# Kernel tuning notes

Hardware: AMD Instinct MI355X
Metric: run time of the kernel (lower is better)

Reference implementation:

```python
import jax, jax.numpy as jnp
import numpy as np
from jax import lax

B, h, Ch = 16, 8, 32
HW = 56
N = HW * HW
SPLITS = [64, 96, 96]  # [2*Ch, 3*Ch, 3*Ch] for windows {3,5,7}


def _dwconv(x, w, b, pad):
    # x: [B, C, H, W]; w: [C, 1, k, k] depthwise (feature_group_count=C)
    y = lax.conv_general_dilated(
        x, w, window_strides=(1, 1), padding=[(pad, pad), (pad, pad)],
        feature_group_count=x.shape[1],
        dimension_numbers=('NCHW', 'OIHW', 'NCHW'))
    return y + b[None, :, None, None]


def setup_inputs() -> dict:
    key = jax.random.key(0)
    ks = jax.random.split(key, 6)
    return {
        'q': jax.random.normal(ks[0], (B, h, N, Ch), dtype=jnp.float32),
        'v': jax.random.normal(ks[1], (B, h, N, Ch), dtype=jnp.float32),
        'w3': jax.random.normal(ks[2], (64, 1, 3, 3), dtype=jnp.float32) * 0.1,
        'b3': jnp.zeros((64,), dtype=jnp.float32),
        'w5': jax.random.normal(ks[3], (96, 1, 5, 5), dtype=jnp.float32) * 0.1,
        'b5': jnp.zeros((96,), dtype=jnp.float32),
        'w7': jax.random.normal(ks[4], (96, 1, 7, 7), dtype=jnp.float32) * 0.1,
        'b7': jnp.zeros((96,), dtype=jnp.float32),
        'H': HW,
        'W': HW,
    }


def reference(q, v, w3, b3, w5, b5, w7, b7, H, W):
    # q, v: [B, h, N, Ch]; N == H*W, Nv == N (same-resolution path, no interpolation)
    Bq, hh, Nq, C = q.shape
    # v: B h (H W) Ch -> B (h*Ch) H W
    v_img = jnp.transpose(v, (0, 1, 3, 2)).reshape(Bq, hh * C, H, W)
    v1, v2, v3 = jnp.split(v_img, np.cumsum(SPLITS)[:-1], axis=1)
    conv_v = jnp.concatenate([
        _dwconv(v1, w3, b3, 1),
        _dwconv(v2, w5, b5, 2),
        _dwconv(v3, w7, b7, 3),
    ], axis=1)  # [B, h*Ch, H, W]
    # B (h*Ch) H W -> B h (H W) Ch
    conv_v = conv_v.reshape(Bq, hh, C, H * W).transpose(0, 1, 3, 2)
    ev = q * conv_v  # [B, h, N, Ch]
    # transpose(1,2).flatten(2): [B, N, h*Ch]
    return jnp.transpose(ev, (0, 2, 1, 3)).reshape(Bq, Nq, hh * C)
```

## Files before the change

### kernel.cpp

```cpp
#include <hip/hip_runtime.h>
#include <cstddef>


#define BH 16
#define NH 8
#define CH 32
#define HW 56
#define NN (HW*HW)
#define ROWB (HW*CH*4)
#define RS 58
#define NROWS_MAX 20
#define BUF_PX (3 + NROWS_MAX*RS + 1)
#define BUF_FLOATS (BUF_PX*CH)

typedef float f32x4 __attribute__((ext_vector_type(4)));
typedef unsigned int u32x4 __attribute__((ext_vector_type(4)));

__device__ __forceinline__ f32x4 bload(__amdgpu_buffer_rsrc_t rs, int voff) {
    u32x4 u = __builtin_amdgcn_raw_buffer_load_b128(rs, voff, 0, 0);
    f32x4 f; __builtin_memcpy(&f, &u, 16); return f;
}

template<int K, int R>
__device__ __forceinline__ void conv_rows(
    const float* __restrict__ q, float* __restrict__ out,
    const float* __restrict__ bias,
    int b, int hh, int y0, int sw, int cbase,
    const float* __restrict__ w_lds, const float* __restrict__ bufs,
    int lane)
{
    constexpr int P  = K / 2;
    constexpr int NR = 7 + K - 1;
    const int xseg = lane >> 3;
    const int chq  = lane & 7;
    const int x0   = xseg * 7;
    const int ch   = chq * 4;

    const float mL = (xseg == 0) ? 0.f : 1.f;
    const float mR = (xseg == 7) ? 0.f : 1.f;

    const f32x4 bias4 = *(const f32x4*)(bias + cbase + ch);
    f32x4 acc[R][7];
#pragma unroll
    for (int u = 0; u < R; ++u)
#pragma unroll
        for (int i = 0; i < 7; ++i) acc[u][i] = bias4;

    for (int rr = 0; rr < R + 2 * P; ++rr) {
        const float* rb = bufs + (size_t)((3 - P + x0) + (sw + rr) * RS) * CH + ch;
        f32x4 r[NR];
#pragma unroll
        for (int j = 0; j < NR; ++j)
            r[j] = *(const f32x4*)(rb + j * CH);
        if constexpr (K == 7) { r[0] *= mL; r[NR - 1] *= mR; }

#pragma unroll
        for (int u = 0; u < R; ++u) {
            const int dy = rr - u;
            if ((unsigned)dy < (unsigned)K) {
#pragma unroll
                for (int dx = 0; dx < K; ++dx) {
                    const f32x4 w4 = *(const f32x4*)(w_lds + (dy * K + dx) * CH + ch);
#pragma unroll
                    for (int i = 0; i < 7; ++i)
                        acc[u][i] += r[i + dx] * w4;
                }
            }
        }
    }

    const size_t plane = ((size_t)b * NH + hh) * (size_t)NN * CH;
#pragma unroll
    for (int u = 0; u < R; ++u) {
        const int y = y0 + sw + u;
        const float* qrow = q + plane + (size_t)y * (HW * CH);
        float* obase = out + ((size_t)b * NN + (size_t)y * HW) * (NH * CH) + hh * CH + ch;
#pragma unroll
        for (int i = 0; i < 7; ++i) {
            const int px = x0 + i;
            const f32x4 q4 = *(const f32x4*)(qrow + (size_t)px * CH + ch);
            const f32x4 o  = acc[u][i] * q4;
            __builtin_nontemporal_store(o, (f32x4*)(obase + (size_t)px * (NH * CH)));
        }
    }
}

template<int K>
__device__ __forceinline__ void run_head(
    const float* __restrict__ q, const float* __restrict__ v,
    const float* __restrict__ w, const float* __restrict__ bias,
    float* __restrict__ out, int b, int hh, int y0, int cbase,
    float* __restrict__ w_lds, float* __restrict__ bufs)
{
    constexpr int P = K / 2;
    constexpr int NROWS = 14 + 2 * P;
    constexpr int NS = (NROWS + 3) / 4;
    const int t = threadIdx.x;

    const int nw = K * K * CH;
    for (int i = t; i < nw; i += 256) {
        int tap = i >> 5, c = i & 31;
        w_lds[tap * CH + c] = w[(cbase + c) * (K * K) + tap];
    }

    {
        f32x4 z = {0.f, 0.f, 0.f, 0.f};
        const int NG = 3 + 2 * NROWS + 1;
        for (int i = t; i < NG * 8; i += 256) {
            const int g = i >> 3, sub = i & 7;
            int px;
            if (g < 3) px = g;
            else if (g < 3 + 2 * NROWS) {
                const int s = (g - 3) >> 1;
                px = 3 + s * RS + 56 + ((g - 3) & 1);
            } else px = 3 + NROWS * RS;
            *(f32x4*)(bufs + (size_t)px * CH + sub * 4) = z;
        }
    }

    const int wid  = t >> 6;
    const int lane = t & 63;
    const size_t plane = ((size_t)b * NH + hh) * (size_t)NN * CH;
    const float* vb = v + plane;

    f32x4 ld[NS][7];
#pragma unroll
    for (int n = 0; n < NS; ++n) {
        const int s = wid + n * 4;
        if (s < NROWS) {
            const int gy = y0 - P + s;
            const bool ok = (unsigned)gy < (unsigned)HW;
            __amdgpu_buffer_rsrc_t rs = __builtin_amdgcn_make_buffer_rsrc(
                (void*)(vb + (ptrdiff_t)gy * (HW * CH)), (short)0, ok ? ROWB : 0, 0x00020000);
#pragma unroll
            for (int k = 0; k < 7; ++k) ld[n][k] = bload(rs, k * 1024 + lane * 16);
        }
    }
#pragma unroll
    for (int n = 0; n < NS; ++n) {
        const int s = wid + n * 4;
        if (s < NROWS) {
            float* dst = bufs + (size_t)(3 + s * RS) * CH;
#pragma unroll
            for (int k = 0; k < 7; ++k)
                *(f32x4*)(dst + k * 256 + lane * 4) = ld[n][k];
        }
    }
    __syncthreads();

    if      (wid == 0) conv_rows<K, 4>(q, out, bias, b, hh, y0, 0,  cbase, w_lds, bufs, lane);
    else if (wid == 1) conv_rows<K, 3>(q, out, bias, b, hh, y0, 4,  cbase, w_lds, bufs, lane);
    else if (wid == 2) conv_rows<K, 3>(q, out, bias, b, hh, y0, 7,  cbase, w_lds, bufs, lane);
    else               conv_rows<K, 4>(q, out, bias, b, hh, y0, 10, cbase, w_lds, bufs, lane);
}

__global__ __launch_bounds__(256, 1)
void clusterformer_fused(const float* __restrict__ q, const float* __restrict__ v,
                         const float* __restrict__ w3, const float* __restrict__ b3,
                         const float* __restrict__ w5, const float* __restrict__ b5,
                         const float* __restrict__ w7, const float* __restrict__ b7,
                         float* __restrict__ out)
{
    __shared__ __align__(16) float bufs[BUF_FLOATS];
    __shared__ __align__(16) float w_lds[49 * CH];

    const int bid  = blockIdx.x;
    const int p_lo = bid & 7;
    const int t2   = bid >> 3;
    const int p_hi = t2 >> 2;
    const int yg   = t2 & 3;
    const int p    = p_hi * 8 + p_lo;
    const int b    = p & 15;
    const int hhp  = p >> 4;
    const int hh   = (hhp < 3) ? (5 + hhp) : ((hhp < 6) ? (hhp - 1) : (hhp - 6));
    const int y0   = yg * 14;

    if (hh < 2)      run_head<3>(q, v, w3, b3, out, b, hh, y0, hh * 32,       w_lds, bufs);
    else if (hh < 5) run_head<5>(q, v, w5, b5, out, b, hh, y0, hh * 32 - 64,  w_lds, bufs);
    else             run_head<7>(q, v, w7, b7, out, b, hh, y0, hh * 32 - 160, w_lds, bufs);
}

extern "C" void kernel_launch(void* const* d_in, const int* in_sizes, int n_in,
                              void* d_out, int out_size, void* d_ws, size_t ws_size,
                              hipStream_t stream) {
    const float* q  = (const float*)d_in[0];
    const float* v  = (const float*)d_in[1];
    const float* w3 = (const float*)d_in[2];
    const float* b3 = (const float*)d_in[3];
    const float* w5 = (const float*)d_in[4];
    const float* b5 = (const float*)d_in[5];
    const float* w7 = (const float*)d_in[6];
    const float* b7 = (const float*)d_in[7];
    float* out = (float*)d_out;

    const int grid = BH * NH * 4;
    clusterformer_fused<<<grid, 256, 0, stream>>>(q, v, w3, b3, w5, b5, w7, b7, out);
}
```

Baseline: 166.0 us.

## Split halo staging into two phases so convolution overlaps remaining row loads

The first 13 input rows are staged to LDS and the rows that depend only on them are convolved, while the remaining halo rows stay in flight in registers. Those rows are written to LDS after a second lightweight barrier. Work is now split as one output row per iteration interleaved across waves instead of contiguous multi-row blocks per wave. This gives up vertical register reuse of loaded rows, so there are more LDS reads, and the output stores are now regular rather than nontemporal. The aim is to hide global load latency behind compute, at the cost of higher register pressure from keeping loads pending.

After: 164.0 us. Within noise of the previous version (-1.2%).

```diff
diff --git a/kernel.cpp b/kernel.cpp
--- a/kernel.cpp
+++ b/kernel.cpp
@@ -21,33 +21,39 @@
     f32x4 f; __builtin_memcpy(&f, &u, 16); return f;
 }
 
-template<int K, int R>
-__device__ __forceinline__ void conv_rows(
+__device__ __forceinline__ void softbar() {
+    asm volatile("s_waitcnt lgkmcnt(0)" ::: "memory");
+    __builtin_amdgcn_s_barrier();
+    __builtin_amdgcn_sched_barrier(0);
+}
+
+template<int K>
+__device__ __forceinline__ void conv_row(
     const float* __restrict__ q, float* __restrict__ out,
-    const float* __restrict__ bias,
-    int b, int hh, int y0, int sw, int cbase,
+    f32x4 bias4, int b, int hh, int y0, int y, int cbase,
     const float* __restrict__ w_lds, const float* __restrict__ bufs,
-    int lane)
+    int x0, int ch, float mL, float mR)
 {
     constexpr int P  = K / 2;
     constexpr int NR = 7 + K - 1;
-    const int xseg = lane >> 3;
-    const int chq  = lane & 7;
-    const int x0   = xseg * 7;
-    const int ch   = chq * 4;
-
-    const float mL = (xseg == 0) ? 0.f : 1.f;
-    const float mR = (xseg == 7) ? 0.f : 1.f;
-
-    const f32x4 bias4 = *(const f32x4*)(bias + cbase + ch);
-    f32x4 acc[R][7];
-#pragma unroll
-    for (int u = 0; u < R; ++u)
-#pragma unroll
-        for (int i = 0; i < 7; ++i) acc[u][i] = bias4;
-
-    for (int rr = 0; rr < R + 2 * P; ++rr) {
-        const float* rb = bufs + (size_t)((3 - P + x0) + (sw + rr) * RS) * CH + ch;
+
+    const size_t plane = ((size_t)b * NH + hh) * (size_t)NN * CH;
+    const int gy = y0 + y;
+    const float* qrow = q + plane + (size_t)gy * (HW * CH);
+
+    f32x4 qf[7];
+#pragma unroll
+    for (int i = 0; i < 7; ++i)
+        qf[i] = *(const f32x4*)(qrow + (size_t)(x0 + i) * CH + ch);
+
+    f32x4 acc[7];
+#pragma unroll
+    for (int i = 0; i < 7; ++i) acc[i] = bias4;
+
+#pragma unroll
+    for (int dy = 0; dy < K; ++dy) {
+        const int s = y + dy;
+        const float* rb = bufs + (size_t)((3 - P + x0) + s * RS) * CH + ch;
         f32x4 r[NR];
 #pragma unroll
         for (int j = 0; j < NR; ++j)
@@ -55,34 +61,18 @@
         if constexpr (K == 7) { r[0] *= mL; r[NR - 1] *= mR; }
 
 #pragma unroll
-        for (int u = 0; u < R; ++u) {
-            const int dy = rr - u;
-            if ((unsigned)dy < (unsigned)K) {
-#pragma unroll
-                for (int dx = 0; dx < K; ++dx) {
-                    const f32x4 w4 = *(const f32x4*)(w_lds + (dy * K + dx) * CH + ch);
-#pragma unroll
-                    for (int i = 0; i < 7; ++i)
-                        acc[u][i] += r[i + dx] * w4;
-                }
-            }
-        }
-    }
-
-    const size_t plane = ((size_t)b * NH + hh) * (size_t)NN * CH;
-#pragma unroll
-    for (int u = 0; u < R; ++u) {
-        const int y = y0 + sw + u;
-        const float* qrow = q + plane + (size_t)y * (HW * CH);
-        float* obase = out + ((size_t)b * NN + (size_t)y * HW) * (NH * CH) + hh * CH + ch;
-#pragma unroll
-        for (int i = 0; i < 7; ++i) {
-            const int px = x0 + i;
-            const f32x4 q4 = *(const f32x4*)(qrow + (size_t)px * CH + ch);
-            const f32x4 o  = acc[u][i] * q4;
-            __builtin_nontemporal_store(o, (f32x4*)(obase + (size_t)px * (NH * CH)));
-        }
-    }
+        for (int dx = 0; dx < K; ++dx) {
+            const f32x4 w4 = *(const f32x4*)(w_lds + (dy * K + dx) * CH + ch);
+#pragma unroll
+            for (int i = 0; i < 7; ++i)
+                acc[i] += r[i + dx] * w4;
+        }
+    }
+
+    float* obase = out + ((size_t)b * NN + (size_t)gy * HW) * (NH * CH) + hh * CH + ch;
+#pragma unroll
+    for (int i = 0; i < 7; ++i)
+        *(f32x4*)(obase + (size_t)(x0 + i) * (NH * CH)) = acc[i] * qf[i];
 }
 
 template<int K>
@@ -94,7 +84,6 @@
 {
     constexpr int P = K / 2;
     constexpr int NROWS = 14 + 2 * P;
-    constexpr int NS = (NROWS + 3) / 4;
     const int t = threadIdx.x;
 
     const int nw = K * K * CH;
@@ -120,38 +109,82 @@
 
     const int wid  = t >> 6;
     const int lane = t & 63;
+    const int xseg = lane >> 3;
+    const int chq  = lane & 7;
+    const int x0   = xseg * 7;
+    const int ch   = chq * 4;
+    const float mL = (xseg == 0) ? 0.f : 1.f;
+    const float mR = (xseg == 7) ? 0.f : 1.f;
+
     const size_t plane = ((size_t)b * NH + hh) * (size_t)NN * CH;
     const float* vb = v + plane;
 
-    f32x4 ld[NS][7];
-#pragma unroll
-    for (int n = 0; n < NS; ++n) {
-        const int s = wid + n * 4;
+    f32x4 ld1[4][7];
+#pragma unroll
+    for (int k = 0; k < 4; ++k) {
+        const int s = wid + 4 * k;
+        if (s <= 12) {
+            const int gy = y0 - P + s;
+            const bool ok = (unsigned)gy < (unsigned)HW;
+            __amdgpu_buffer_rsrc_t rs = __builtin_amdgcn_make_buffer_rsrc(
+                (void*)(vb + (ptrdiff_t)gy * (HW * CH)), (short)0, ok ? ROWB : 0, 0x00020000);
+#pragma unroll
+            for (int j = 0; j < 7; ++j) ld1[k][j] = bload(rs, j * 1024 + lane * 16);
+        }
+    }
+    f32x4 ld2[2][7];
+    const int s2b = 13 + ((wid + 3) & 3);
+#pragma unroll
+    for (int k = 0; k < 2; ++k) {
+        const int s = s2b + 4 * k;
         if (s < NROWS) {
             const int gy = y0 - P + s;
             const bool ok = (unsigned)gy < (unsigned)HW;
             __amdgpu_buffer_rsrc_t rs = __builtin_amdgcn_make_buffer_rsrc(
                 (void*)(vb + (ptrdiff_t)gy * (HW * CH)), (short)0, ok ? ROWB : 0, 0x00020000);
 #pragma unroll
-            for (int k = 0; k < 7; ++k) ld[n][k] = bload(rs, k * 1024 + lane * 16);
-        }
-    }
-#pragma unroll
-    for (int n = 0; n < NS; ++n) {
-        const int s = wid + n * 4;
+            for (int j = 0; j < 7; ++j) ld2[k][j] = bload(rs, j * 1024 + lane * 16);
+        }
+    }
+#pragma unroll
+    for (int k = 0; k < 4; ++k) {
+        const int s = wid + 4 * k;
+        if (s <= 12) {
+            float* dst = bufs + (size_t)(3 + s * RS) * CH;
+#pragma unroll
+            for (int j = 0; j < 7; ++j)
+                *(f32x4*)(dst + j * 256 + lane * 4) = ld1[k][j];
+        }
+    }
+    softbar();
+
+    const f32x4 bias4 = *(const f32x4*)(bias + cbase + ch);
+
+#pragma unroll
+    for (int u = 0; u < 4; ++u) {
+        const int y = wid + 4 * u;
+        if (y < 14 && y + 2 * P <= 12)
+            conv_row<K>(q, out, bias4, b, hh, y0, y, cbase, w_lds, bufs, x0, ch, mL, mR);
+    }
+
+#pragma unroll
+    for (int k = 0; k < 2; ++k) {
+        const int s = s2b + 4 * k;
         if (s < NROWS) {
             float* dst = bufs + (size_t)(3 + s * RS) * CH;
 #pragma unroll
-            for (int k = 0; k < 7; ++k)
-                *(f32x4*)(dst + k * 256 + lane * 4) = ld[n][k];
-        }
-    }
-    __syncthreads();
-
-    if      (wid == 0) conv_rows<K, 4>(q, out, bias, b, hh, y0, 0,  cbase, w_lds, bufs, lane);
-    else if (wid == 1) conv_rows<K, 3>(q, out, bias, b, hh, y0, 4,  cbase, w_lds, bufs, lane);
-    else if (wid == 2) conv_rows<K, 3>(q, out, bias, b, hh, y0, 7,  cbase, w_lds, bufs, lane);
-    else               conv_rows<K, 4>(q, out, bias, b, hh, y0, 10, cbase, w_lds, bufs, lane);
+            for (int j = 0; j < 7; ++j)
+                *(f32x4*)(dst + j * 256 + lane * 4) = ld2[k][j];
+        }
+    }
+    softbar();
+
+#pragma unroll
+    for (int u = 0; u < 4; ++u) {
+        const int y = wid + 4 * u;
+        if (y < 14 && y + 2 * P > 12)
+            conv_row<K>(q, out, bias4, b, hh, y0, y, cbase, w_lds, bufs, x0, ch, mL, mR);
+    }
 }
 
 __global__ __launch_bounds__(256, 1)
```
